# Kernel optimization log

Measured on AMD Instinct MI355X. Metric: run time of the kernel, lower is better.

## Reference

```python
import jax, jax.numpy as jnp
import numpy as np

B, H, N = 128, 512, 1024

def setup_inputs() -> dict:
    key = jax.random.key(0)
    ks = jax.random.split(key, 9)
    s = 1.0 / np.sqrt(H)
    return {
        "mc_hidden": jax.random.normal(ks[0], (B, H), jnp.float32),
        "sn_hidden": jax.random.normal(ks[1], (B, H, N), jnp.float32),
        "attn_W": jax.random.normal(ks[2], (H, 2 * H), jnp.float32) * s,
        "attn_v": jax.random.normal(ks[3], (H,), jnp.float32) * s,
        "ptr_v": jax.random.normal(ks[4], (H,), jnp.float32) * s,
        "fc1_W": jax.random.normal(ks[5], (H, 2 * H), jnp.float32) * s,
        "fc1_b": jax.random.normal(ks[6], (H,), jnp.float32) * s,
        "fc2_W": jax.random.normal(ks[7], (H, H), jnp.float32) * s,
        "fc2_b": jax.random.normal(ks[8], (H,), jnp.float32) * s,
    }


def reference(mc_hidden, sn_hidden, attn_W, attn_v, ptr_v, fc1_W, fc1_b, fc2_W, fc2_b):
    # ---- Attention (Bahdanau-style additive scoring) ----
    # hidden: (B, 2H, N) = cat(sn_hidden, mc expanded along N) on dim 1
    mc_exp = jnp.broadcast_to(mc_hidden[:, :, None], sn_hidden.shape)  # (B,H,N)
    hidden = jnp.concatenate((sn_hidden, mc_exp), axis=1)              # (B,2H,N)
    # W @ hidden -> (B,H,N); v @ tanh(.) -> (B,N)
    scores = jnp.einsum('h,bhn->bn', attn_v,
                        jnp.tanh(jnp.einsum('hk,bkn->bhn', attn_W, hidden)))
    attns = jax.nn.softmax(scores, axis=-1)                            # (B,N)
    # ---- Context + pointer scoring ----
    context = jnp.einsum('bn,bhn->bh', attns, sn_hidden)               # (B,H)
    x = jnp.concatenate((mc_hidden, context), axis=1)                  # (B,2H)
    out = jax.nn.relu(x @ fc1_W.T + fc1_b)                             # (B,H)
    out = jax.nn.relu(out @ fc2_W.T + fc2_b)                           # (B,H)
    probs = jnp.einsum('h,bhn->bn', ptr_v,
                       jnp.tanh(sn_hidden + out[:, :, None]))          # (B,N)
    return probs
```

## Files before the change

### kernel.cpp

```cpp
#include <hip/hip_runtime.h>
#include <hip/hip_bf16.h>

#define Bn 128
#define Hd 512
#define Nn 1024

typedef __attribute__((ext_vector_type(8))) short short8;
typedef __attribute__((ext_vector_type(4))) float f32x4;

__device__ __forceinline__ unsigned short f2bf(float f) {
    unsigned x;
    __builtin_memcpy(&x, &f, 4);
    unsigned r = x + 0x7fffu + ((x >> 16) & 1u);
    return (unsigned short)(r >> 16);
}

__device__ __forceinline__ float wave_sum(float v) {
    v += __shfl_xor(v, 32);
    v += __shfl_xor(v, 16);
    v += __shfl_xor(v, 8);
    v += __shfl_xor(v, 4);
    v += __shfl_xor(v, 2);
    v += __shfl_xor(v, 1);
    return v;
}

__device__ __forceinline__ float tanh_fast(float x) {
    float e = __expf(2.0f * x);
    return 1.0f - 2.0f / (e + 1.0f);
}

__global__ void convert_W_kernel(const float* __restrict__ attn_W,
                                 unsigned short* __restrict__ Wb) {
    int idx = (blockIdx.x * 256 + threadIdx.x) * 8;
    int h = idx >> 9;
    int k = idx & 511;
    const float* p = attn_W + (size_t)h * 1024 + k;
    float4 v0 = *(const float4*)p;
    float4 v1 = *(const float4*)(p + 4);
    unsigned short t[8] = {f2bf(v0.x), f2bf(v0.y), f2bf(v0.z), f2bf(v0.w),
                           f2bf(v1.x), f2bf(v1.y), f2bf(v1.z), f2bf(v1.w)};
    *(uint4*)(Wb + idx) = *(uint4*)t;
}

__global__ void mc_term_kernel(const float* __restrict__ mc,
                               const float* __restrict__ attn_W,
                               float* __restrict__ mc_term) {
    int wg = (blockIdx.x * blockDim.x + threadIdx.x) >> 6;
    int lane = threadIdx.x & 63;
    int b = wg >> 9;
    int h = wg & 511;
    const float* m = mc + b * Hd + lane * 8;
    const float* w = attn_W + (size_t)h * 1024 + 512 + lane * 8;
    float4 m0 = *(const float4*)m, m1 = *(const float4*)(m + 4);
    float4 w0 = *(const float4*)w, w1 = *(const float4*)(w + 4);
    float acc = m0.x * w0.x + m0.y * w0.y + m0.z * w0.z + m0.w * w0.w +
                m1.x * w1.x + m1.y * w1.y + m1.z * w1.z + m1.w * w1.w;
    acc = wave_sum(acc);
    if (lane == 0) mc_term[b * Hd + h] = acc;
}

__global__ __launch_bounds__(256, 2)
void attn_score_kernel(const float* __restrict__ sn,
                       const unsigned short* __restrict__ Wb,
                       const float* __restrict__ attn_v,
                       const float* __restrict__ mc_term,
                       float* __restrict__ scores) {
    __shared__ __align__(16) unsigned short snT[64][72];
    __shared__ float av_s[512];
    __shared__ float mct_s[512];
    __shared__ float ssum[64];

    const int b = blockIdx.x >> 4;
    const int n0 = (blockIdx.x & 15) * 64;
    const int tid = threadIdx.x;
    const int lane = tid & 63;
    const int wid = tid >> 6;
    const int quad = lane >> 4;
    const int l15 = lane & 15;
    const int m0 = wid * 128;

    av_s[tid] = attn_v[tid];
    av_s[tid + 256] = attn_v[tid + 256];
    mct_s[tid] = mc_term[b * Hd + tid];
    mct_s[tid + 256] = mc_term[b * Hd + tid + 256];

    f32x4 acc[8][4];
#pragma unroll
    for (int i = 0; i < 8; ++i)
#pragma unroll
        for (int j = 0; j < 4; ++j) {
            f32x4 z = {0.f, 0.f, 0.f, 0.f};
            acc[i][j] = z;
        }

    const short* W = (const short*)Wb;

    for (int k0 = 0; k0 < 512; k0 += 64) {
#pragma unroll
        for (int j = 0; j < 2; ++j) {
            int c = tid + j * 256;
            int n = c & 63;
            int kb = (c >> 6) * 8;
            const float* p = sn + ((size_t)(b * Hd + k0 + kb)) * Nn + n0 + n;
            unsigned short t[8];
#pragma unroll
            for (int i = 0; i < 8; ++i) t[i] = f2bf(p[(size_t)i * Nn]);
            *(uint4*)&snT[n][kb] = *(uint4*)t;
        }
        __syncthreads();
#pragma unroll
        for (int kk = 0; kk < 64; kk += 32) {
            short8 bfr[4];
#pragma unroll
            for (int nt = 0; nt < 4; ++nt)
                bfr[nt] = *(const short8*)&snT[nt * 16 + l15][kk + quad * 8];
#pragma unroll
            for (int mt = 0; mt < 8; ++mt) {
                const short8 aw =
                    *(const short8*)(W + (size_t)(m0 + mt * 16 + l15) * 512 + k0 + kk + quad * 8);
#pragma unroll
                for (int nt = 0; nt < 4; ++nt)
                    acc[mt][nt] = __builtin_amdgcn_mfma_f32_16x16x32_bf16(aw, bfr[nt], acc[mt][nt], 0, 0, 0);
            }
        }
        __syncthreads();
    }

    float s[4] = {0.f, 0.f, 0.f, 0.f};
#pragma unroll
    for (int mt = 0; mt < 8; ++mt) {
        int hb = m0 + mt * 16 + quad * 4;
#pragma unroll
        for (int r = 0; r < 4; ++r) {
            float av = av_s[hb + r];
            float mcv = mct_s[hb + r];
#pragma unroll
            for (int nt = 0; nt < 4; ++nt)
                s[nt] += av * tanh_fast(acc[mt][nt][r] + mcv);
        }
    }
    if (tid < 64) ssum[tid] = 0.f;
    __syncthreads();
#pragma unroll
    for (int nt = 0; nt < 4; ++nt) {
        float v = s[nt];
        v += __shfl_xor(v, 16);
        v += __shfl_xor(v, 32);
        if (lane < 16) atomicAdd(&ssum[nt * 16 + l15], v);
    }
    __syncthreads();
    if (tid < 64) scores[b * Nn + n0 + tid] = ssum[tid];
}

__global__ void softmax_kernel(float* __restrict__ scores) {
    const int b = blockIdx.x;
    const int tid = threadIdx.x;
    const int lane = tid & 63, wid = tid >> 6;
    __shared__ float red[4];
    float v[4];
#pragma unroll
    for (int i = 0; i < 4; ++i) v[i] = scores[b * Nn + tid + i * 256];
    float m = fmaxf(fmaxf(v[0], v[1]), fmaxf(v[2], v[3]));
#pragma unroll
    for (int off = 32; off >= 1; off >>= 1) m = fmaxf(m, __shfl_xor(m, off));
    if (lane == 0) red[wid] = m;
    __syncthreads();
    m = fmaxf(fmaxf(red[0], red[1]), fmaxf(red[2], red[3]));
    __syncthreads();
    float s = 0.f;
#pragma unroll
    for (int i = 0; i < 4; ++i) {
        v[i] = __expf(v[i] - m);
        s += v[i];
    }
    s = wave_sum(s);
    if (lane == 0) red[wid] = s;
    __syncthreads();
    s = red[0] + red[1] + red[2] + red[3];
    float inv = 1.0f / s;
#pragma unroll
    for (int i = 0; i < 4; ++i) scores[b * Nn + tid + i * 256] = v[i] * inv;
}

__global__ void context_kernel(const float* __restrict__ sn,
                               const float* __restrict__ attns,
                               float* __restrict__ context) {
    int wg = (blockIdx.x * blockDim.x + threadIdx.x) >> 6;
    int lane = threadIdx.x & 63;
    int b = wg >> 9, h = wg & 511;
    const float* row = sn + ((size_t)(b * Hd + h)) * Nn;
    const float* at = attns + b * Nn;
    float acc = 0.f;
#pragma unroll
    for (int i = 0; i < 2; ++i) {
        int n = i * 512 + lane * 8;
        float4 s0 = *(const float4*)(row + n);
        float4 s1 = *(const float4*)(row + n + 4);
        float4 a0 = *(const float4*)(at + n);
        float4 a1 = *(const float4*)(at + n + 4);
        acc += s0.x * a0.x + s0.y * a0.y + s0.z * a0.z + s0.w * a0.w;
        acc += s1.x * a1.x + s1.y * a1.y + s1.z * a1.z + s1.w * a1.w;
    }
    acc = wave_sum(acc);
    if (lane == 0) context[b * Hd + h] = acc;
}

__global__ void fc1_kernel(const float* __restrict__ mc,
                           const float* __restrict__ ctx,
                           const float* __restrict__ fc1_W,
                           const float* __restrict__ fc1_b,
                           float* __restrict__ out1) {
    int wg = (blockIdx.x * blockDim.x + threadIdx.x) >> 6;
    int lane = threadIdx.x & 63;
    int b = wg >> 9, h = wg & 511;
    const float* wr = fc1_W + (size_t)h * 1024;
    float acc = 0.f;
    {
        float4 w0 = *(const float4*)(wr + lane * 8);
        float4 w1 = *(const float4*)(wr + lane * 8 + 4);
        float4 x0 = *(const float4*)(mc + b * Hd + lane * 8);
        float4 x1 = *(const float4*)(mc + b * Hd + lane * 8 + 4);
        acc += w0.x * x0.x + w0.y * x0.y + w0.z * x0.z + w0.w * x0.w;
        acc += w1.x * x1.x + w1.y * x1.y + w1.z * x1.z + w1.w * x1.w;
    }
    {
        float4 w0 = *(const float4*)(wr + 512 + lane * 8);
        float4 w1 = *(const float4*)(wr + 512 + lane * 8 + 4);
        float4 x0 = *(const float4*)(ctx + b * Hd + lane * 8);
        float4 x1 = *(const float4*)(ctx + b * Hd + lane * 8 + 4);
        acc += w0.x * x0.x + w0.y * x0.y + w0.z * x0.z + w0.w * x0.w;
        acc += w1.x * x1.x + w1.y * x1.y + w1.z * x1.z + w1.w * x1.w;
    }
    acc = wave_sum(acc);
    if (lane == 0) out1[b * Hd + h] = fmaxf(acc + fc1_b[h], 0.f);
}

__global__ void fc2_kernel(const float* __restrict__ out1,
                           const float* __restrict__ fc2_W,
                           const float* __restrict__ fc2_b,
                           float* __restrict__ out2) {
    int wg = (blockIdx.x * blockDim.x + threadIdx.x) >> 6;
    int lane = threadIdx.x & 63;
    int b = wg >> 9, h = wg & 511;
    const float* wr = fc2_W + (size_t)h * 512 + lane * 8;
    float4 w0 = *(const float4*)wr;
    float4 w1 = *(const float4*)(wr + 4);
    float4 x0 = *(const float4*)(out1 + b * Hd + lane * 8);
    float4 x1 = *(const float4*)(out1 + b * Hd + lane * 8 + 4);
    float acc = w0.x * x0.x + w0.y * x0.y + w0.z * x0.z + w0.w * x0.w +
                w1.x * x1.x + w1.y * x1.y + w1.z * x1.z + w1.w * x1.w;
    acc = wave_sum(acc);
    if (lane == 0) out2[b * Hd + h] = fmaxf(acc + fc2_b[h], 0.f);
}

__global__ void final_kernel(const float* __restrict__ sn,
                             const float* __restrict__ ptr_v,
                             const float* __restrict__ out2,
                             float* __restrict__ probs) {
    const int b = blockIdx.x >> 1;
    const int n0 = (blockIdx.x & 1) * 512;
    const int tid = threadIdx.x;
    __shared__ float pv_s[512], o2_s[512];
    pv_s[tid] = ptr_v[tid];
    pv_s[tid + 256] = ptr_v[tid + 256];
    o2_s[tid] = out2[b * Hd + tid];
    o2_s[tid + 256] = out2[b * Hd + tid + 256];
    __syncthreads();
    const float* base = sn + (size_t)b * Hd * Nn + n0 + tid * 2;
    float a0 = 0.f, a1 = 0.f;
#pragma unroll 8
    for (int h = 0; h < 512; ++h) {
        float2 d = *(const float2*)(base + (size_t)h * Nn);
        float o = o2_s[h], w = pv_s[h];
        a0 += w * tanh_fast(d.x + o);
        a1 += w * tanh_fast(d.y + o);
    }
    float* op = probs + b * Nn + n0 + tid * 2;
    op[0] = a0;
    op[1] = a1;
}

extern "C" void kernel_launch(void* const* d_in, const int* in_sizes, int n_in,
                              void* d_out, int out_size, void* d_ws, size_t ws_size,
                              hipStream_t stream) {
    const float* mc  = (const float*)d_in[0];
    const float* sn  = (const float*)d_in[1];
    const float* aW  = (const float*)d_in[2];
    const float* av  = (const float*)d_in[3];
    const float* pv  = (const float*)d_in[4];
    const float* f1W = (const float*)d_in[5];
    const float* f1b = (const float*)d_in[6];
    const float* f2W = (const float*)d_in[7];
    const float* f2b = (const float*)d_in[8];

    unsigned short* Wb = (unsigned short*)d_ws;
    float* fws = (float*)(Wb + 512 * 512);
    float* mc_term = fws;
    float* scores  = mc_term + Bn * Hd;
    float* context = scores + Bn * Nn;
    float* out1    = context + Bn * Hd;
    float* out2    = out1 + Bn * Hd;
    float* probs   = (float*)d_out;

    convert_W_kernel<<<dim3(128), dim3(256), 0, stream>>>(aW, Wb);
    mc_term_kernel<<<dim3(16384), dim3(256), 0, stream>>>(mc, aW, mc_term);
    attn_score_kernel<<<dim3(2048), dim3(256), 0, stream>>>(sn, Wb, av, mc_term, scores);
    softmax_kernel<<<dim3(128), dim3(256), 0, stream>>>(scores);
    context_kernel<<<dim3(16384), dim3(256), 0, stream>>>(sn, scores, context);
    fc1_kernel<<<dim3(16384), dim3(256), 0, stream>>>(mc, context, f1W, f1b, out1);
    fc2_kernel<<<dim3(16384), dim3(256), 0, stream>>>(out1, f2W, f2b, out2);
    final_kernel<<<dim3(256), dim3(256), 0, stream>>>(sn, pv, out2, probs);
}
```

Measured before the change: 630.8 us.

## Pre-transpose sn to bf16 once and reuse it in attention, context and final

A new kernel converts sn_hidden into a bf16 buffer with N-major, H-contiguous layout. The attention GEMM, context reduction and final tanh pass all read this half-size buffer instead of re-reading fp32 sn. The GEMM drops its LDS staging and loads fragments directly from global memory. Context now splits N across blocks and combines partial sums with atomics after a memset, and division is replaced by rcp. The cost is an extra full pass over sn plus a large workspace, and context and final now use bf16-rounded sn, which adds precision error.

```diff
diff --git a/kernel.cpp b/kernel.cpp
--- a/kernel.cpp
+++ b/kernel.cpp
@@ -7,6 +7,13 @@
 
 typedef __attribute__((ext_vector_type(8))) short short8;
 typedef __attribute__((ext_vector_type(4))) float f32x4;
+
+__device__ __forceinline__ float bf2f(unsigned u) {
+    unsigned v = u << 16;
+    float f;
+    __builtin_memcpy(&f, &v, 4);
+    return f;
+}
 
 __device__ __forceinline__ unsigned short f2bf(float f) {
     unsigned x;
@@ -27,7 +34,7 @@
 
 __device__ __forceinline__ float tanh_fast(float x) {
     float e = __expf(2.0f * x);
-    return 1.0f - 2.0f / (e + 1.0f);
+    return 1.0f - 2.0f * __builtin_amdgcn_rcpf(e + 1.0f);
 }
 
 __global__ void convert_W_kernel(const float* __restrict__ attn_W,
@@ -41,6 +48,24 @@
     unsigned short t[8] = {f2bf(v0.x), f2bf(v0.y), f2bf(v0.z), f2bf(v0.w),
                            f2bf(v1.x), f2bf(v1.y), f2bf(v1.z), f2bf(v1.w)};
     *(uint4*)(Wb + idx) = *(uint4*)t;
+}
+
+__global__ void transpose_sn_kernel(const float* __restrict__ sn,
+                                    unsigned short* __restrict__ snT) {
+    int bidx = blockIdx.x;
+    int b = bidx >> 7;
+    int kt = (bidx >> 4) & 7;
+    int nt = bidx & 15;
+    int k0 = kt << 6, n0 = nt << 6;
+    int t = threadIdx.x;
+    int n = t >> 2, kp = t & 3;
+    const float* src = sn + ((size_t)(b * Hd) + k0 + kp * 16) * Nn + n0 + n;
+    unsigned short tmp[16];
+#pragma unroll
+    for (int j = 0; j < 16; ++j) tmp[j] = f2bf(src[(size_t)j * Nn]);
+    unsigned short* dst = snT + ((size_t)(b * Nn) + n0 + n) * Hd + k0 + kp * 16;
+    *(uint4*)dst = *(uint4*)tmp;
+    *(uint4*)(dst + 8) = *(uint4*)(tmp + 8);
 }
 
 __global__ void mc_term_kernel(const float* __restrict__ mc,
@@ -61,18 +86,17 @@
 }
 
 __global__ __launch_bounds__(256, 2)
-void attn_score_kernel(const float* __restrict__ sn,
+void attn_score_kernel(const unsigned short* __restrict__ snT,
                        const unsigned short* __restrict__ Wb,
                        const float* __restrict__ attn_v,
                        const float* __restrict__ mc_term,
                        float* __restrict__ scores) {
-    __shared__ __align__(16) unsigned short snT[64][72];
     __shared__ float av_s[512];
     __shared__ float mct_s[512];
     __shared__ float ssum[64];
 
     const int b = blockIdx.x >> 4;
-    const int n0 = (blockIdx.x & 15) * 64;
+    const int n0 = (blockIdx.x & 15) << 6;
     const int tid = threadIdx.x;
     const int lane = tid & 63;
     const int wid = tid >> 6;
@@ -94,38 +118,26 @@
             acc[i][j] = z;
         }
 
-    const short* W = (const short*)Wb;
-
-    for (int k0 = 0; k0 < 512; k0 += 64) {
-#pragma unroll
-        for (int j = 0; j < 2; ++j) {
-            int c = tid + j * 256;
-            int n = c & 63;
-            int kb = (c >> 6) * 8;
-            const float* p = sn + ((size_t)(b * Hd + k0 + kb)) * Nn + n0 + n;
-            unsigned short t[8];
-#pragma unroll
-            for (int i = 0; i < 8; ++i) t[i] = f2bf(p[(size_t)i * Nn]);
-            *(uint4*)&snT[n][kb] = *(uint4*)t;
-        }
-        __syncthreads();
-#pragma unroll
-        for (int kk = 0; kk < 64; kk += 32) {
-            short8 bfr[4];
+    const short* Abase = (const short*)Wb + (size_t)(m0 + l15) * Hd + quad * 8;
+    const short* Bbase = (const short*)snT + ((size_t)(b * Nn) + n0 + l15) * Hd + quad * 8;
+
+#pragma unroll 2
+    for (int k0 = 0; k0 < 512; k0 += 32) {
+        short8 bfr[4], aw[8];
+#pragma unroll
+        for (int nt = 0; nt < 4; ++nt)
+            bfr[nt] = *(const short8*)(Bbase + (size_t)(nt * 16) * Hd + k0);
+#pragma unroll
+        for (int mt = 0; mt < 8; ++mt)
+            aw[mt] = *(const short8*)(Abase + (size_t)(mt * 16) * Hd + k0);
+#pragma unroll
+        for (int mt = 0; mt < 8; ++mt)
 #pragma unroll
             for (int nt = 0; nt < 4; ++nt)
-                bfr[nt] = *(const short8*)&snT[nt * 16 + l15][kk + quad * 8];
-#pragma unroll
-            for (int mt = 0; mt < 8; ++mt) {
-                const short8 aw =
-                    *(const short8*)(W + (size_t)(m0 + mt * 16 + l15) * 512 + k0 + kk + quad * 8);
-#pragma unroll
-                for (int nt = 0; nt < 4; ++nt)
-                    acc[mt][nt] = __builtin_amdgcn_mfma_f32_16x16x32_bf16(aw, bfr[nt], acc[mt][nt], 0, 0, 0);
-            }
-        }
-        __syncthreads();
-    }
+                acc[mt][nt] = __builtin_amdgcn_mfma_f32_16x16x32_bf16(aw[mt], bfr[nt], acc[mt][nt], 0, 0, 0);
+    }
+
+    __syncthreads();
 
     float s[4] = {0.f, 0.f, 0.f, 0.f};
 #pragma unroll
@@ -178,32 +190,31 @@
     if (lane == 0) red[wid] = s;
     __syncthreads();
     s = red[0] + red[1] + red[2] + red[3];
-    float inv = 1.0f / s;
+    float inv = __builtin_amdgcn_rcpf(s);
 #pragma unroll
     for (int i = 0; i < 4; ++i) scores[b * Nn + tid + i * 256] = v[i] * inv;
 }
 
-__global__ void context_kernel(const float* __restrict__ sn,
+__global__ void context_kernel(const unsigned short* __restrict__ snT,
                                const float* __restrict__ attns,
                                float* __restrict__ context) {
-    int wg = (blockIdx.x * blockDim.x + threadIdx.x) >> 6;
-    int lane = threadIdx.x & 63;
-    int b = wg >> 9, h = wg & 511;
-    const float* row = sn + ((size_t)(b * Hd + h)) * Nn;
-    const float* at = attns + b * Nn;
-    float acc = 0.f;
-#pragma unroll
-    for (int i = 0; i < 2; ++i) {
-        int n = i * 512 + lane * 8;
-        float4 s0 = *(const float4*)(row + n);
-        float4 s1 = *(const float4*)(row + n + 4);
-        float4 a0 = *(const float4*)(at + n);
-        float4 a1 = *(const float4*)(at + n + 4);
-        acc += s0.x * a0.x + s0.y * a0.y + s0.z * a0.z + s0.w * a0.w;
-        acc += s1.x * a1.x + s1.y * a1.y + s1.z * a1.z + s1.w * a1.w;
-    }
-    acc = wave_sum(acc);
-    if (lane == 0) context[b * Hd + h] = acc;
+    int b = blockIdx.x >> 3;
+    int nc = (blockIdx.x & 7) << 7;
+    int t = threadIdx.x;
+    __shared__ float a_s[128];
+    if (t < 128) a_s[t] = attns[b * Nn + nc + t];
+    __syncthreads();
+    const unsigned short* base = snT + ((size_t)(b * Nn) + nc) * Hd + t * 2;
+    float acc0 = 0.f, acc1 = 0.f;
+#pragma unroll 4
+    for (int i = 0; i < 128; ++i) {
+        unsigned d = *(const unsigned*)(base + (size_t)i * Hd);
+        float a = a_s[i];
+        acc0 += a * bf2f(d & 0xffffu);
+        acc1 += a * bf2f(d >> 16);
+    }
+    atomicAdd(&context[b * Hd + 2 * t], acc0);
+    atomicAdd(&context[b * Hd + 2 * t + 1], acc1);
 }
 
 __global__ void fc1_kernel(const float* __restrict__ mc,
@@ -254,31 +265,39 @@
     if (lane == 0) out2[b * Hd + h] = fmaxf(acc + fc2_b[h], 0.f);
 }
 
-__global__ void final_kernel(const float* __restrict__ sn,
+__global__ void final_kernel(const unsigned short* __restrict__ snT,
                              const float* __restrict__ ptr_v,
                              const float* __restrict__ out2,
                              float* __restrict__ probs) {
-    const int b = blockIdx.x >> 1;
-    const int n0 = (blockIdx.x & 1) * 512;
-    const int tid = threadIdx.x;
+    int b = blockIdx.x >> 4;
+    int n0 = (blockIdx.x & 15) << 6;
+    int t = threadIdx.x;
+    int n = n0 + (t >> 2), p = t & 3;
     __shared__ float pv_s[512], o2_s[512];
-    pv_s[tid] = ptr_v[tid];
-    pv_s[tid + 256] = ptr_v[tid + 256];
-    o2_s[tid] = out2[b * Hd + tid];
-    o2_s[tid + 256] = out2[b * Hd + tid + 256];
-    __syncthreads();
-    const float* base = sn + (size_t)b * Hd * Nn + n0 + tid * 2;
-    float a0 = 0.f, a1 = 0.f;
-#pragma unroll 8
-    for (int h = 0; h < 512; ++h) {
-        float2 d = *(const float2*)(base + (size_t)h * Nn);
-        float o = o2_s[h], w = pv_s[h];
-        a0 += w * tanh_fast(d.x + o);
-        a1 += w * tanh_fast(d.y + o);
-    }
-    float* op = probs + b * Nn + n0 + tid * 2;
-    op[0] = a0;
-    op[1] = a1;
+    pv_s[t] = ptr_v[t];
+    pv_s[t + 256] = ptr_v[t + 256];
+    o2_s[t] = out2[b * Hd + t];
+    o2_s[t + 256] = out2[b * Hd + t + 256];
+    __syncthreads();
+    const unsigned short* row = snT + ((size_t)(b * Nn) + n) * Hd + p * 8;
+    float a = 0.f;
+#pragma unroll 4
+    for (int j = 0; j < 16; ++j) {
+        uint4 d = *(const uint4*)(row + j * 32);
+        int hb = p * 8 + j * 32;
+        const unsigned* u = (const unsigned*)&d;
+#pragma unroll
+        for (int q = 0; q < 4; ++q) {
+            int h = hb + q * 2;
+            float x0 = bf2f(u[q] & 0xffffu);
+            float x1 = bf2f(u[q] >> 16);
+            a += pv_s[h] * tanh_fast(x0 + o2_s[h]);
+            a += pv_s[h + 1] * tanh_fast(x1 + o2_s[h + 1]);
+        }
+    }
+    a += __shfl_xor(a, 1);
+    a += __shfl_xor(a, 2);
+    if (p == 0) probs[b * Nn + n] = a;
 }
 
 extern "C" void kernel_launch(void* const* d_in, const int* in_sizes, int n_in,
@@ -294,8 +313,9 @@
     const float* f2W = (const float*)d_in[7];
     const float* f2b = (const float*)d_in[8];
 
-    unsigned short* Wb = (unsigned short*)d_ws;
-    float* fws = (float*)(Wb + 512 * 512);
+    unsigned short* snT = (unsigned short*)d_ws;
+    unsigned short* Wb  = snT + (size_t)Bn * Nn * Hd;
+    float* fws     = (float*)(Wb + 512 * 512);
     float* mc_term = fws;
     float* scores  = mc_term + Bn * Hd;
     float* context = scores + Bn * Nn;
@@ -303,12 +323,14 @@
     float* out2    = out1 + Bn * Hd;
     float* probs   = (float*)d_out;
 
+    hipMemsetAsync(context, 0, Bn * Hd * sizeof(float), stream);
     convert_W_kernel<<<dim3(128), dim3(256), 0, stream>>>(aW, Wb);
+    transpose_sn_kernel<<<dim3(16384), dim3(256), 0, stream>>>(sn, snT);
     mc_term_kernel<<<dim3(16384), dim3(256), 0, stream>>>(mc, aW, mc_term);
-    attn_score_kernel<<<dim3(2048), dim3(256), 0, stream>>>(sn, Wb, av, mc_term, scores);
+    attn_score_kernel<<<dim3(2048), dim3(256), 0, stream>>>(snT, Wb, av, mc_term, scores);
     softmax_kernel<<<dim3(128), dim3(256), 0, stream>>>(scores);
-    context_kernel<<<dim3(16384), dim3(256), 0, stream>>>(sn, scores, context);
+    context_kernel<<<dim3(1024), dim3(256), 0, stream>>>(snT, scores, context);
     fc1_kernel<<<dim3(16384), dim3(256), 0, stream>>>(mc, context, f1W, f1b, out1);
     fc2_kernel<<<dim3(16384), dim3(256), 0, stream>>>(out1, f2W, f2b, out2);
-    final_kernel<<<dim3(256), dim3(256), 0, stream>>>(sn, pv, out2, probs);
-}
+    final_kernel<<<dim3(2048), dim3(256), 0, stream>>>(snT, pv, out2, probs);
+}
```

New measurement: 672.2 us. +6.6%, slower.
